# Kernel tuning notes

Measured on AMD Instinct MI355X. Metric: run time of the kernel, lower is better.

## Reference

```python
import jax, jax.numpy as jnp
import numpy as np

L, B, S, H, NH, DH, I, MAXP, NL = 4, 8, 512, 1024, 32, 32, 4096, 512, 20
EPS = 1e-12


def setup_inputs() -> dict:
    key = jax.random.key(0)
    ks = jax.random.split(key, 12)
    sc = 0.02
    w = lambda k, shape: jax.random.normal(k, shape, jnp.float32) * sc
    p = {}
    p['hidden_states'] = jax.random.normal(ks[0], (B, S, H), jnp.float32)
    p['attention_mask'] = jnp.ones((B, S), jnp.float32)
    p['Wq'] = w(ks[1], (L, H, H)); p['bq'] = jnp.zeros((L, H), jnp.float32)
    p['Wk'] = w(ks[2], (L, H, H)); p['bk'] = jnp.zeros((L, H), jnp.float32)
    p['Wv'] = w(ks[3], (L, H, H)); p['bv'] = jnp.zeros((L, H), jnp.float32)
    p['Wo'] = w(ks[4], (L, H, H)); p['bo'] = jnp.zeros((L, H), jnp.float32)
    p['ln1_g'] = jnp.ones((L, H), jnp.float32); p['ln1_b'] = jnp.zeros((L, H), jnp.float32)
    p['W1'] = w(ks[5], (L, H, I)); p['b1'] = jnp.zeros((L, I), jnp.float32)
    p['W2'] = w(ks[6], (L, I, H)); p['b2'] = jnp.zeros((L, H), jnp.float32)
    p['ln2_g'] = jnp.ones((L, H), jnp.float32); p['ln2_b'] = jnp.zeros((L, H), jnp.float32)
    p['rel_emb'] = w(ks[7], (L, 2 * MAXP - 1, DH))
    p['pool_W'] = w(ks[8], (3 * H, H)); p['pool_b'] = jnp.zeros((H,), jnp.float32)
    p['pool_ln_g'] = jnp.ones((H,), jnp.float32); p['pool_ln_b'] = jnp.zeros((H,), jnp.float32)
    p['cls_W'] = w(ks[9], (H, NL)); p['cls_b'] = jnp.zeros((NL,), jnp.float32)
    return p


def _ln(x, g, b):
    mu = jnp.mean(x, -1, keepdims=True)
    var = jnp.mean(jnp.square(x - mu), -1, keepdims=True)
    return (x - mu) * jax.lax.rsqrt(var + EPS) * g + b


def reference(hidden_states, attention_mask, Wq, bq, Wk, bk, Wv, bv, Wo, bo,
              ln1_g, ln1_b, W1, b1, W2, b2, ln2_g, ln2_b, rel_emb,
              pool_W, pool_b, pool_ln_g, pool_ln_b, cls_W, cls_b):
    b, s, h = hidden_states.shape
    # extended additive attention mask (0 -> -1e9)
    mask_add = (1.0 - attention_mask)[:, None, None, :] * -1e9
    pos = jnp.arange(s)
    rel_idx = pos[:, None] - pos[None, :] + MAXP - 1  # [s, s] in [0, 2*MAXP-2]
    x = hidden_states
    for l in range(L):
        heads = lambda t: t.reshape(b, s, NH, DH).transpose(0, 2, 1, 3)
        q = heads(x @ Wq[l] + bq[l])
        k = heads(x @ Wk[l] + bk[l])
        v = heads(x @ Wv[l] + bv[l])
        # learned relative-position bias; note head_size == num_heads by construction
        rel = rel_emb[l][rel_idx].transpose(2, 0, 1)  # [DH==NH, s, s]
        scores = jnp.einsum('bhqd,bhkd->bhqk', q, k) + rel[None]
        scores = scores / np.float32(np.sqrt(DH)) + mask_add
        probs = jax.nn.softmax(scores, axis=-1)
        ctx = jnp.einsum('bhqk,bhkd->bhqd', probs, v).transpose(0, 2, 1, 3).reshape(b, s, h)
        x = _ln(ctx @ Wo[l] + bo[l] + x, ln1_g[l], ln1_b[l])
        inner = jax.nn.gelu(x @ W1[l] + b1[l], approximate=False) @ W2[l] + b2[l]
        x = _ln(x + inner, ln2_g[l], ln2_b[l])
    # AdvancedPooling: mean + max + first token
    m = attention_mask[..., None]
    mean_pool = jnp.sum(x * m, axis=1) / jnp.sum(attention_mask, axis=1, keepdims=True)
    max_pool = jnp.max(x + (1.0 - m) * -1e9, axis=1)
    pooled = jnp.concatenate([mean_pool, max_pool, x[:, 0]], axis=-1)
    pooled = _ln(pooled @ pool_W + pool_b, pool_ln_g, pool_ln_b)
    return pooled @ cls_W + cls_b
```

## Files before the change

kernel.cpp:

```cpp
#include <hip/hip_runtime.h>
#include <math.h>

typedef __attribute__((ext_vector_type(8))) _Float16 f16x8;
typedef __attribute__((ext_vector_type(4))) float f32x4;

__device__ __forceinline__ ushort f2h(float x) {
  union { _Float16 h; ushort u; } c;
  c.h = (_Float16)x;
  return c.u;
}
__device__ __forceinline__ void gl_lds16(const ushort* g, ushort* l) {
  __builtin_amdgcn_global_load_lds(
      (const __attribute__((address_space(1))) unsigned int*)g,
      (__attribute__((address_space(3))) unsigned int*)l, 16, 0, 0);
}
__device__ __forceinline__ f32x4 mfma16(f16x8 a, f16x8 b, f32x4 c) {
  return __builtin_amdgcn_mfma_f32_16x16x32_f16(a, b, c, 0, 0, 0);
}

__device__ __forceinline__ float block_reduce_sum(float v, float* sb) {
#pragma unroll
  for (int o = 32; o > 0; o >>= 1) v += __shfl_down(v, o, 64);
  const int t = threadIdx.x;
  if ((t & 63) == 0) sb[t >> 6] = v;
  __syncthreads();
  v = sb[0] + sb[1] + sb[2] + sb[3];
  __syncthreads();
  return v;
}

__global__ __launch_bounds__(256) void acast(const float* __restrict__ X,
                                             ushort* __restrict__ H, int n4) {
  const int i = blockIdx.x * 256 + threadIdx.x;
  if (i >= n4) return;
  const float4 x = ((const float4*)X)[i];
  ushort4 h;
  h.x = f2h(x.x); h.y = f2h(x.y); h.z = f2h(x.z); h.w = f2h(x.w);
  ((ushort4*)H)[i] = h;
}

__global__ __launch_bounds__(256) void concat3(const float* __restrict__ a,
                                               const float* __restrict__ b,
                                               const float* __restrict__ c,
                                               float* __restrict__ o) {
  const int i = blockIdx.x * 256 + threadIdx.x;
  o[i] = i < 1024 ? a[i] : (i < 2048 ? b[i - 1024] : c[i - 2048]);
}

__global__ __launch_bounds__(256) void wcast_t(const float* __restrict__ W,
                                               ushort* __restrict__ T,
                                               int K, int N) {
  __shared__ float s[32][33];
  const int tx = threadIdx.x & 31, ty = threadIdx.x >> 5;
  const int n0 = blockIdx.x * 32, k0 = blockIdx.y * 32;
#pragma unroll
  for (int i = 0; i < 4; ++i)
    s[ty + i * 8][tx] = W[(size_t)(k0 + ty + i * 8) * N + n0 + tx];
  __syncthreads();
#pragma unroll
  for (int i = 0; i < 4; ++i) {
    const int n = ty + i * 8;
    T[(size_t)(n0 + n) * K + k0 + tx] = f2h(s[tx][n]);
  }
}

template <int EPI, int NF>
__global__ __launch_bounds__(256, NF == 4 ? 2 : 3) void gemm_mfma(
    const ushort* __restrict__ A, const ushort* __restrict__ B,
    const float* __restrict__ bias, const float* __restrict__ res,
    float* __restrict__ C, ushort* __restrict__ O, int M, int N, int K) {
  __shared__ __align__(16) ushort sA[2][4096], sB[2][NF * 1024];
  const int t = threadIdx.x, w = t >> 6, lane = t & 63;
  const int llo = lane & 15, lhi = lane >> 4;
  const int wm = w >> 1, wn = w & 1;

  const int gx = gridDim.x;
  int wg = blockIdx.y * gx + blockIdx.x;
  const int nwg = gx * gridDim.y;
  wg = (wg & 7) * (nwg >> 3) + (wg >> 3);
  const int bm = (wg / gx) * 128, bn = (wg % gx) * (NF * 32);

  const ushort* pA0 = A + (size_t)(bm + lane) * K + w * 8;
  const ushort* pA1 = pA0 + (size_t)64 * K;
  const ushort* pB0 = B + (size_t)(bn + lane) * K + w * 8;
  const ushort* pB1 = (NF == 4) ? pB0 + (size_t)64 * K : pB0;

  auto STAGE = [&](int buf, int k0) {
    gl_lds16(pA0 + k0, &sA[buf][w * 1024]);
    gl_lds16(pA1 + k0, &sA[buf][w * 1024 + 512]);
    if (NF == 4) {
      gl_lds16(pB0 + k0, &sB[buf][w * 1024]);
      gl_lds16(pB1 + k0, &sB[buf][w * 1024 + 512]);
    } else {
      gl_lds16(pB0 + k0, &sB[buf][w * 512]);
    }
  };

  f32x4 acc[4][NF] = {};
  const int NT = K >> 5;
  STAGE(0, 0);
  __syncthreads();
  int cur = 0;
  for (int kt = 0; kt < NT; ++kt) {
    if (kt + 1 < NT) STAGE(cur ^ 1, (kt + 1) << 5);
    f16x8 a[4], bf[NF];
#pragma unroll
    for (int f = 0; f < 4; ++f)
      a[f] = *(const f16x8*)&sA[cur][lhi * 1024 + (wm * 64 + f * 16 + llo) * 8];
#pragma unroll
    for (int f = 0; f < NF; ++f)
      bf[f] = *(const f16x8*)&sB[cur][lhi * (NF * 256) +
                                      (wn * (NF * 16) + f * 16 + llo) * 8];
#pragma unroll
    for (int fm = 0; fm < 4; ++fm)
#pragma unroll
      for (int fn = 0; fn < NF; ++fn)
        acc[fm][fn] = mfma16(a[fm], bf[fn], acc[fm][fn]);
    __syncthreads();
    cur ^= 1;
  }

#pragma unroll
  for (int fm = 0; fm < 4; ++fm) {
    const int row0 = bm + wm * 64 + fm * 16 + lhi * 4;
#pragma unroll
    for (int fn = 0; fn < NF; ++fn) {
      const int col = bn + wn * (NF * 16) + fn * 16 + llo;
      const float bc = bias[col];
      if (EPI == 5) {
        if (col < 2048) {
          const size_t base = (size_t)(col >> 10) * (4096 * 1024) + (col & 1023);
#pragma unroll
          for (int r = 0; r < 4; ++r)
            O[base + (size_t)(row0 + r) * 1024] = f2h(acc[fm][fn][r] + bc);
        } else {
          const int c = col - 2048;
          ushort4 vh;
#pragma unroll
          for (int r = 0; r < 4; ++r) ((ushort*)&vh)[r] = f2h(acc[fm][fn][r] + bc);
          const size_t o = (size_t)8 * 1024 * 1024 +
              ((size_t)(((row0 >> 9) * 32 + (c >> 5)) * 32 + (c & 31))) * 512 +
              (row0 & 511);
          *(ushort4*)(O + o) = vh;
        }
      } else {
#pragma unroll
        for (int r = 0; r < 4; ++r) {
          const size_t o = (size_t)(row0 + r) * N + col;
          float v = acc[fm][fn][r] + bc;
          if (EPI == 2) {
            v += res[o];
            C[o] = v;
          } else {
            v = 0.5f * v * (1.f + erff(v * 0.70710678118654752f));
            O[o] = f2h(v);
          }
        }
      }
    }
  }
}

__global__ __launch_bounds__(512, 2) void attn_mfma(
    const ushort* __restrict__ Qg, const ushort* __restrict__ Kg,
    const ushort* __restrict__ Vg, const float* __restrict__ mask,
    const float* __restrict__ rel_l, ushort* __restrict__ Cg) {
  __shared__ __align__(16) ushort sK[16384], sV[16384];
  __shared__ __align__(16) ushort sP[5120];
  __shared__ float rel_s[1024];
  __shared__ float madd[512];

  const int h = blockIdx.x, b = blockIdx.y, z = blockIdx.z;
  const int t = threadIdx.x, w = t >> 6, lane = t & 63;
  const int llo = lane & 15, lhi = lane >> 4;
  const float SCALE = 0.17677669529663687f;

#pragma unroll
  for (int it = 0; it < 4; ++it) {
    const int task = t + it * 512;
    const int s = task >> 2, oct = task & 3;
    const size_t g = (size_t)(b * 512 + s) * 1024 + h * 32 + oct * 8;
    *(uint4*)&sK[oct * 4096 + s * 8] = *(const uint4*)(Kg + g);
  }
#pragma unroll
  for (int it = 0; it < 4; ++it) {
    const int task = t + it * 512;
    const int d = task >> 6, ko = task & 63;
    const size_t g = (size_t)((b * 32 + h) * 32 + d) * 512 + ko * 8;
    *(uint4*)&sV[ko * 256 + d * 8] = *(const uint4*)(Vg + g);
  }
  for (int i = t; i < 1023; i += 512) rel_s[i] = rel_l[(size_t)i * 32 + h];
  for (int i = t; i < 512; i += 512) madd[i] = (1.f - mask[b * 512 + i]) * -1e9f;
  __syncthreads();

  uint* wP = (uint*)(sP + w * 640 + llo * 40);
  const ushort* rP = sP + w * 640 + llo * 40;

  for (int qt = 0; qt < 2; ++qt) {
    const int q = z * 256 + w * 32 + qt * 16 + llo;
    const size_t qg = (size_t)(b * 512 + q) * 1024 + h * 32 + lhi * 8;
    const f16x8 fQ = *(const f16x8*)(Qg + qg);
    float m = -INFINITY, l = 0.f;
    f32x4 acc0 = {0.f, 0.f, 0.f, 0.f};
    f32x4 acc1 = {0.f, 0.f, 0.f, 0.f};

    for (int kt2 = 0; kt2 < 16; ++kt2) {
      float p[8];
      float tm = -INFINITY;
#pragma unroll
      for (int sub = 0; sub < 2; ++sub) {
        const int kt = kt2 * 2 + sub;
        const f16x8 fK = *(const f16x8*)&sK[lhi * 4096 + (kt * 16 + llo) * 8];
        f32x4 s4 = {0.f, 0.f, 0.f, 0.f};
        s4 = mfma16(fK, fQ, s4);
#pragma unroll
        for (int r = 0; r < 4; ++r) {
          const int k = kt * 16 + lhi * 4 + r;
          const float sv = (s4[r] + rel_s[q - k + 511]) * SCALE + madd[k];
          p[sub * 4 + r] = sv;
          tm = fmaxf(tm, sv);
        }
      }
      tm = fmaxf(tm, __shfl_xor(tm, 16));
      tm = fmaxf(tm, __shfl_xor(tm, 32));
      const float nm = fmaxf(m, tm);
      const float sc = __expf(m - nm);
      float ts = 0.f;
#pragma unroll
      for (int i = 0; i < 8; ++i) {
        p[i] = __expf(p[i] - nm);
        ts += p[i];
      }
      ts += __shfl_xor(ts, 16);
      ts += __shfl_xor(ts, 32);
      l = l * sc + ts;
      m = nm;
      acc0 *= sc;
      acc1 *= sc;
#pragma unroll
      for (int sub = 0; sub < 2; ++sub) {
        wP[sub * 8 + lhi * 2 + 0] =
            (uint)f2h(p[sub * 4 + 0]) | ((uint)f2h(p[sub * 4 + 1]) << 16);
        wP[sub * 8 + lhi * 2 + 1] =
            (uint)f2h(p[sub * 4 + 2]) | ((uint)f2h(p[sub * 4 + 3]) << 16);
      }
      const f16x8 fP = *(const f16x8*)(rP + lhi * 8);
      const int vb = (kt2 * 4 + lhi) * 256;
      const f16x8 fV0 = *(const f16x8*)&sV[vb + llo * 8];
      const f16x8 fV1 = *(const f16x8*)&sV[vb + (16 + llo) * 8];
      acc0 = mfma16(fV0, fP, acc0);
      acc1 = mfma16(fV1, fP, acc1);
    }

    const float invl = 1.f / l;
    const size_t ob = (size_t)(b * 512 + q) * 1024 + h * 32;
    ushort4 oh;
#pragma unroll
    for (int r = 0; r < 4; ++r) ((ushort*)&oh)[r] = f2h(acc0[r] * invl);
    *(ushort4*)(Cg + ob + lhi * 4) = oh;
#pragma unroll
    for (int r = 0; r < 4; ++r) ((ushort*)&oh)[r] = f2h(acc1[r] * invl);
    *(ushort4*)(Cg + ob + 16 + lhi * 4) = oh;
  }
}

__global__ __launch_bounds__(256) void ln_kernel(
    const float* __restrict__ X, const float* __restrict__ g,
    const float* __restrict__ bt, float* __restrict__ out,
    ushort* __restrict__ O) {
  __shared__ float sb[4];
  const int row = blockIdx.x, t = threadIdx.x;
  const float4 x = *(const float4*)&X[(size_t)row * 1024 + t * 4];
  const float s = block_reduce_sum(x.x + x.y + x.z + x.w, sb);
  const float mu = s * (1.f / 1024.f);
  const float dx = x.x - mu, dy = x.y - mu, dz = x.z - mu, dw = x.w - mu;
  const float ss = block_reduce_sum(dx * dx + dy * dy + dz * dz + dw * dw, sb);
  const float rs = rsqrtf(ss * (1.f / 1024.f) + 1e-12f);
  const float4 gv = *(const float4*)&g[t * 4];
  const float4 bv = *(const float4*)&bt[t * 4];
  float4 o;
  o.x = dx * rs * gv.x + bv.x;
  o.y = dy * rs * gv.y + bv.y;
  o.z = dz * rs * gv.z + bv.z;
  o.w = dw * rs * gv.w + bv.w;
  *(float4*)&out[(size_t)row * 1024 + t * 4] = o;
  if (O) {
    ushort4 vh;
    vh.x = f2h(o.x); vh.y = f2h(o.y); vh.z = f2h(o.z); vh.w = f2h(o.w);
    *(ushort4*)&O[(size_t)row * 1024 + t * 4] = vh;
  }
}

__global__ __launch_bounds__(128) void pool_kernel(
    const float* __restrict__ X, const float* __restrict__ mask,
    float* __restrict__ pooled) {
  const int b = blockIdx.y;
  const int col = blockIdx.x * 128 + threadIdx.x;
  float sum = 0.f, mx = -INFINITY, cnt = 0.f;
  for (int s = 0; s < 512; ++s) {
    const float v = X[(size_t)(b * 512 + s) * 1024 + col];
    const float mk = mask[b * 512 + s];
    sum = fmaf(v, mk, sum);
    cnt += mk;
    mx = fmaxf(mx, v + (1.f - mk) * -1e9f);
  }
  pooled[(size_t)b * 3072 + col] = sum / cnt;
  pooled[(size_t)b * 3072 + 1024 + col] = mx;
  pooled[(size_t)b * 3072 + 2048 + col] = X[(size_t)(b * 512) * 1024 + col];
}

__global__ __launch_bounds__(256) void pool_gemm_kernel(
    const float* __restrict__ P, const float* __restrict__ W,
    const float* __restrict__ bias, float* __restrict__ out) {
  const int idx = blockIdx.x * 256 + threadIdx.x;
  const int b = idx >> 10, n = idx & 1023;
  const float* pr = P + (size_t)b * 3072;
  float a = 0.f;
  for (int k = 0; k < 3072; ++k) a = fmaf(pr[k], W[(size_t)k * 1024 + n], a);
  out[idx] = a + bias[n];
}

__global__ __launch_bounds__(64) void cls_kernel(
    const float* __restrict__ X, const float* __restrict__ W,
    const float* __restrict__ bias, float* __restrict__ out) {
  const int b = blockIdx.x, n = threadIdx.x;
  if (n < 20) {
    float a = 0.f;
    for (int k = 0; k < 1024; ++k)
      a = fmaf(X[(size_t)b * 1024 + k], W[(size_t)k * 20 + n], a);
    out[b * 20 + n] = a + bias[n];
  }
}

extern "C" void kernel_launch(void* const* d_in, const int* in_sizes, int n_in,
                              void* d_out, int out_size, void* d_ws, size_t ws_size,
                              hipStream_t stream) {
  const float* hs    = (const float*)d_in[0];
  const float* amask = (const float*)d_in[1];
  const float* Wq    = (const float*)d_in[2];
  const float* bq    = (const float*)d_in[3];
  const float* Wk    = (const float*)d_in[4];
  const float* bk    = (const float*)d_in[5];
  const float* Wv    = (const float*)d_in[6];
  const float* bv    = (const float*)d_in[7];
  const float* Wo    = (const float*)d_in[8];
  const float* bo    = (const float*)d_in[9];
  const float* ln1g  = (const float*)d_in[10];
  const float* ln1b  = (const float*)d_in[11];
  const float* W1    = (const float*)d_in[12];
  const float* b1    = (const float*)d_in[13];
  const float* W2    = (const float*)d_in[14];
  const float* b2    = (const float*)d_in[15];
  const float* ln2g  = (const float*)d_in[16];
  const float* ln2b  = (const float*)d_in[17];
  const float* rel   = (const float*)d_in[18];
  const float* poolW = (const float*)d_in[19];
  const float* poolb = (const float*)d_in[20];
  const float* plng  = (const float*)d_in[21];
  const float* plnb  = (const float*)d_in[22];
  const float* clsW  = (const float*)d_in[23];
  const float* clsb  = (const float*)d_in[24];

  char* W = (char*)d_ws;
  const size_t MB = (size_t)1 << 20;
  const size_t QK = (size_t)4096 * 1024;
  const size_t WP = (size_t)1024 * 1024;
  float* buf_t  = (float*)(W + 0 * MB);
  float* buf_h1 = (float*)(W + 16 * MB);
  float* buf_x  = (float*)(W + 32 * MB);
  ushort* PL  = (ushort*)(W + 48 * MB);
  ushort* CTX = (ushort*)(W + 72 * MB);
  ushort* Xp  = CTX;
  ushort* H1  = (ushort*)(W + 80 * MB);
  ushort* F1  = (ushort*)(W + 88 * MB);
  ushort* Wt  = (ushort*)(W + 120 * MB);
  float* bcat = (float*)(W + 126 * MB);
  float* pooled  = (float*)(W + 127 * MB);
  float* pool_h  = pooled + 8 * 3072;
  float* pool_h2 = pool_h + 8 * 1024;

  const int n4act = (4096 * 1024) / 4;
  const dim3 gQKV(3072 / 128, 32);
  const dim3 gN64(1024 / 64, 32);
  const dim3 gF1(4096 / 128, 32);
  const dim3 wsQ(1024 / 32, 1024 / 32);

  acast<<<n4act / 256, 256, 0, stream>>>(hs, Xp, n4act);

  const float* x_in = hs;
  for (int l = 0; l < 4; ++l) {
    const float* Wq_l = Wq + (size_t)l * 1024 * 1024;
    const float* Wk_l = Wk + (size_t)l * 1024 * 1024;
    const float* Wv_l = Wv + (size_t)l * 1024 * 1024;
    const float* Wo_l = Wo + (size_t)l * 1024 * 1024;
    const float* W1_l = W1 + (size_t)l * 1024 * 4096;
    const float* W2_l = W2 + (size_t)l * 4096 * 1024;

    concat3<<<12, 256, 0, stream>>>(bq + l * 1024, bk + l * 1024, bv + l * 1024, bcat);
    wcast_t<<<wsQ, 256, 0, stream>>>(Wq_l, Wt, 1024, 1024);
    wcast_t<<<wsQ, 256, 0, stream>>>(Wk_l, Wt + WP, 1024, 1024);
    wcast_t<<<wsQ, 256, 0, stream>>>(Wv_l, Wt + 2 * WP, 1024, 1024);
    gemm_mfma<5, 4><<<gQKV, 256, 0, stream>>>(Xp, Wt, bcat, nullptr, nullptr,
                                              PL, 4096, 3072, 1024);

    attn_mfma<<<dim3(32, 8, 2), 512, 0, stream>>>(
        PL, PL + QK, PL + 2 * QK, amask, rel + (size_t)l * 1023 * 32, CTX);

    wcast_t<<<wsQ, 256, 0, stream>>>(Wo_l, Wt, 1024, 1024);
    gemm_mfma<2, 2><<<gN64, 256, 0, stream>>>(CTX, Wt, bo + l * 1024, x_in,
                                              buf_t, nullptr, 4096, 1024, 1024);
    ln_kernel<<<4096, 256, 0, stream>>>(buf_t, ln1g + l * 1024, ln1b + l * 1024,
                                        buf_h1, H1);

    wcast_t<<<dim3(4096 / 32, 1024 / 32), 256, 0, stream>>>(W1_l, Wt, 1024, 4096);
    gemm_mfma<1, 4><<<gF1, 256, 0, stream>>>(H1, Wt, b1 + l * 4096, nullptr,
                                             nullptr, F1, 4096, 4096, 1024);
    wcast_t<<<dim3(1024 / 32, 4096 / 32), 256, 0, stream>>>(W2_l, Wt, 4096, 1024);
    gemm_mfma<2, 2><<<gN64, 256, 0, stream>>>(F1, Wt, b2 + l * 1024, buf_h1,
                                              buf_t, nullptr, 4096, 1024, 4096);
    ln_kernel<<<4096, 256, 0, stream>>>(buf_t, ln2g + l * 1024, ln2b + l * 1024,
                                        buf_x, Xp);
    x_in = buf_x;
  }

  pool_kernel<<<dim3(8, 8), 128, 0, stream>>>(buf_x, amask, pooled);
  pool_gemm_kernel<<<32, 256, 0, stream>>>(pooled, poolW, poolb, pool_h);
  ln_kernel<<<8, 256, 0, stream>>>(pool_h, plng, plnb, pool_h2, nullptr);
  cls_kernel<<<8, 64, 0, stream>>>(pool_h2, clsW, clsb, (float*)d_out);
}
```

Measured before the change: 1.611 ms.

## Split-K wide-tile GEMMs, fuse QKV weight casts, parallelize pooling and classifier head

The GEMM kernel now always uses 128x128 tiles, and the N=1024 projections (Wo and W2) use a 2-way K split whose second partial is summed inside the layernorm kernel. The three QKV weight transposes are merged into one launch. The pooling, pooler GEMM and classifier are split across many more threads with partial-reduction kernels, replacing long serial loops. These changes target low parallelism in the tail kernels and tile reuse in the GEMMs, at the cost of extra fp32 partial buffers and more launches.

```diff
diff --git a/kernel.cpp b/kernel.cpp
--- a/kernel.cpp
+++ b/kernel.cpp
@@ -64,58 +64,75 @@
   }
 }
 
-template <int EPI, int NF>
-__global__ __launch_bounds__(256, NF == 4 ? 2 : 3) void gemm_mfma(
+__global__ __launch_bounds__(256) void wcast_t3(const float* __restrict__ W0,
+                                                const float* __restrict__ W1,
+                                                const float* __restrict__ W2,
+                                                ushort* __restrict__ T) {
+  __shared__ float s[32][33];
+  const float* W = blockIdx.z == 0 ? W0 : (blockIdx.z == 1 ? W1 : W2);
+  ushort* Tp = T + (size_t)blockIdx.z * 1024 * 1024;
+  const int tx = threadIdx.x & 31, ty = threadIdx.x >> 5;
+  const int n0 = blockIdx.x * 32, k0 = blockIdx.y * 32;
+#pragma unroll
+  for (int i = 0; i < 4; ++i)
+    s[ty + i * 8][tx] = W[(size_t)(k0 + ty + i * 8) * 1024 + n0 + tx];
+  __syncthreads();
+#pragma unroll
+  for (int i = 0; i < 4; ++i) {
+    const int n = ty + i * 8;
+    Tp[(size_t)(n0 + n) * 1024 + k0 + tx] = f2h(s[tx][n]);
+  }
+}
+
+template <int EPI, int KSPLIT>
+__global__ __launch_bounds__(256, 2) void gemm_mfma(
     const ushort* __restrict__ A, const ushort* __restrict__ B,
     const float* __restrict__ bias, const float* __restrict__ res,
-    float* __restrict__ C, ushort* __restrict__ O, int M, int N, int K) {
-  __shared__ __align__(16) ushort sA[2][4096], sB[2][NF * 1024];
+    float* __restrict__ C, float* __restrict__ C2, ushort* __restrict__ O,
+    int M, int N, int K) {
+  __shared__ __align__(16) ushort sA[2][4096], sB[2][4096];
   const int t = threadIdx.x, w = t >> 6, lane = t & 63;
   const int llo = lane & 15, lhi = lane >> 4;
   const int wm = w >> 1, wn = w & 1;
+  const int z = (KSPLIT > 1) ? blockIdx.z : 0;
+  const int Ks = K / KSPLIT;
 
   const int gx = gridDim.x;
   int wg = blockIdx.y * gx + blockIdx.x;
   const int nwg = gx * gridDim.y;
   wg = (wg & 7) * (nwg >> 3) + (wg >> 3);
-  const int bm = (wg / gx) * 128, bn = (wg % gx) * (NF * 32);
-
-  const ushort* pA0 = A + (size_t)(bm + lane) * K + w * 8;
+  const int bm = (wg / gx) * 128, bn = (wg % gx) * 128;
+
+  const ushort* pA0 = A + (size_t)(bm + lane) * K + w * 8 + z * Ks;
   const ushort* pA1 = pA0 + (size_t)64 * K;
-  const ushort* pB0 = B + (size_t)(bn + lane) * K + w * 8;
-  const ushort* pB1 = (NF == 4) ? pB0 + (size_t)64 * K : pB0;
+  const ushort* pB0 = B + (size_t)(bn + lane) * K + w * 8 + z * Ks;
+  const ushort* pB1 = pB0 + (size_t)64 * K;
 
   auto STAGE = [&](int buf, int k0) {
     gl_lds16(pA0 + k0, &sA[buf][w * 1024]);
     gl_lds16(pA1 + k0, &sA[buf][w * 1024 + 512]);
-    if (NF == 4) {
-      gl_lds16(pB0 + k0, &sB[buf][w * 1024]);
-      gl_lds16(pB1 + k0, &sB[buf][w * 1024 + 512]);
-    } else {
-      gl_lds16(pB0 + k0, &sB[buf][w * 512]);
-    }
+    gl_lds16(pB0 + k0, &sB[buf][w * 1024]);
+    gl_lds16(pB1 + k0, &sB[buf][w * 1024 + 512]);
   };
 
-  f32x4 acc[4][NF] = {};
-  const int NT = K >> 5;
+  f32x4 acc[4][4] = {};
+  const int NT = Ks >> 5;
   STAGE(0, 0);
   __syncthreads();
   int cur = 0;
   for (int kt = 0; kt < NT; ++kt) {
     if (kt + 1 < NT) STAGE(cur ^ 1, (kt + 1) << 5);
-    f16x8 a[4], bf[NF];
-#pragma unroll
-    for (int f = 0; f < 4; ++f)
+    f16x8 a[4], bfr[4];
+#pragma unroll
+    for (int f = 0; f < 4; ++f) {
       a[f] = *(const f16x8*)&sA[cur][lhi * 1024 + (wm * 64 + f * 16 + llo) * 8];
-#pragma unroll
-    for (int f = 0; f < NF; ++f)
-      bf[f] = *(const f16x8*)&sB[cur][lhi * (NF * 256) +
-                                      (wn * (NF * 16) + f * 16 + llo) * 8];
+      bfr[f] = *(const f16x8*)&sB[cur][lhi * 1024 + (wn * 64 + f * 16 + llo) * 8];
+    }
 #pragma unroll
     for (int fm = 0; fm < 4; ++fm)
 #pragma unroll
-      for (int fn = 0; fn < NF; ++fn)
-        acc[fm][fn] = mfma16(a[fm], bf[fn], acc[fm][fn]);
+      for (int fn = 0; fn < 4; ++fn)
+        acc[fm][fn] = mfma16(a[fm], bfr[fn], acc[fm][fn]);
     __syncthreads();
     cur ^= 1;
   }
@@ -124,8 +141,8 @@
   for (int fm = 0; fm < 4; ++fm) {
     const int row0 = bm + wm * 64 + fm * 16 + lhi * 4;
 #pragma unroll
-    for (int fn = 0; fn < NF; ++fn) {
-      const int col = bn + wn * (NF * 16) + fn * 16 + llo;
+    for (int fn = 0; fn < 4; ++fn) {
+      const int col = bn + wn * 64 + fn * 16 + llo;
       const float bc = bias[col];
       if (EPI == 5) {
         if (col < 2048) {
@@ -143,18 +160,22 @@
               (row0 & 511);
           *(ushort4*)(O + o) = vh;
         }
+      } else if (EPI == 2) {
+#pragma unroll
+        for (int r = 0; r < 4; ++r) {
+          const size_t o = (size_t)(row0 + r) * N + col;
+          if (KSPLIT == 1 || z == 0)
+            C[o] = acc[fm][fn][r] + bc + res[o];
+          else
+            C2[o] = acc[fm][fn][r];
+        }
       } else {
 #pragma unroll
         for (int r = 0; r < 4; ++r) {
           const size_t o = (size_t)(row0 + r) * N + col;
           float v = acc[fm][fn][r] + bc;
-          if (EPI == 2) {
-            v += res[o];
-            C[o] = v;
-          } else {
-            v = 0.5f * v * (1.f + erff(v * 0.70710678118654752f));
-            O[o] = f2h(v);
-          }
+          v = 0.5f * v * (1.f + erff(v * 0.70710678118654752f));
+          O[o] = f2h(v);
         }
       }
     }
@@ -265,12 +286,16 @@
 }
 
 __global__ __launch_bounds__(256) void ln_kernel(
-    const float* __restrict__ X, const float* __restrict__ g,
-    const float* __restrict__ bt, float* __restrict__ out,
-    ushort* __restrict__ O) {
+    const float* __restrict__ X, const float* __restrict__ X2,
+    const float* __restrict__ g, const float* __restrict__ bt,
+    float* __restrict__ out, ushort* __restrict__ O) {
   __shared__ float sb[4];
   const int row = blockIdx.x, t = threadIdx.x;
-  const float4 x = *(const float4*)&X[(size_t)row * 1024 + t * 4];
+  float4 x = *(const float4*)&X[(size_t)row * 1024 + t * 4];
+  if (X2) {
+    const float4 y = *(const float4*)&X2[(size_t)row * 1024 + t * 4];
+    x.x += y.x; x.y += y.y; x.z += y.z; x.w += y.w;
+  }
   const float s = block_reduce_sum(x.x + x.y + x.z + x.w, sb);
   const float mu = s * (1.f / 1024.f);
   const float dx = x.x - mu, dy = x.y - mu, dz = x.z - mu, dw = x.w - mu;
@@ -291,45 +316,98 @@
   }
 }
 
-__global__ __launch_bounds__(128) void pool_kernel(
+__global__ __launch_bounds__(128) void pool_part(
     const float* __restrict__ X, const float* __restrict__ mask,
-    float* __restrict__ pooled) {
-  const int b = blockIdx.y;
-  const int col = blockIdx.x * 128 + threadIdx.x;
+    float* __restrict__ psum, float* __restrict__ pmax,
+    float* __restrict__ pcnt) {
+  const int cb = blockIdx.x, b = blockIdx.y, sb = blockIdx.z;
+  const int col = cb * 128 + threadIdx.x;
   float sum = 0.f, mx = -INFINITY, cnt = 0.f;
-  for (int s = 0; s < 512; ++s) {
+  for (int i = 0; i < 128; ++i) {
+    const int s = sb * 128 + i;
     const float v = X[(size_t)(b * 512 + s) * 1024 + col];
     const float mk = mask[b * 512 + s];
     sum = fmaf(v, mk, sum);
     cnt += mk;
     mx = fmaxf(mx, v + (1.f - mk) * -1e9f);
   }
-  pooled[(size_t)b * 3072 + col] = sum / cnt;
-  pooled[(size_t)b * 3072 + 1024 + col] = mx;
+  psum[(size_t)(sb * 8 + b) * 1024 + col] = sum;
+  pmax[(size_t)(sb * 8 + b) * 1024 + col] = mx;
+  if (cb == 0 && threadIdx.x == 0) pcnt[sb * 8 + b] = cnt;
+}
+
+__global__ __launch_bounds__(256) void pool_fin(
+    const float* __restrict__ X, const float* __restrict__ psum,
+    const float* __restrict__ pmax, const float* __restrict__ pcnt,
+    float* __restrict__ pooled) {
+  const int idx = blockIdx.x * 256 + threadIdx.x;
+  const int b = idx >> 10, col = idx & 1023;
+  float s = 0.f, m = -INFINITY, c = 0.f;
+#pragma unroll
+  for (int sb = 0; sb < 4; ++sb) {
+    s += psum[(size_t)(sb * 8 + b) * 1024 + col];
+    m = fmaxf(m, pmax[(size_t)(sb * 8 + b) * 1024 + col]);
+    c += pcnt[sb * 8 + b];
+  }
+  pooled[(size_t)b * 3072 + col] = s / c;
+  pooled[(size_t)b * 3072 + 1024 + col] = m;
   pooled[(size_t)b * 3072 + 2048 + col] = X[(size_t)(b * 512) * 1024 + col];
 }
 
-__global__ __launch_bounds__(256) void pool_gemm_kernel(
+__global__ __launch_bounds__(256) void pgemm_part(
     const float* __restrict__ P, const float* __restrict__ W,
-    const float* __restrict__ bias, float* __restrict__ out) {
+    float* __restrict__ part) {
+  __shared__ float sP[8][192];
+  __shared__ float sacc[256][9];
+  const int nb = blockIdx.x, kb = blockIdx.y;
+  const int t = threadIdx.x;
+  const int k0 = kb * 192, n0 = nb * 64;
+  for (int i = t; i < 1536; i += 256)
+    sP[i / 192][i % 192] = P[(size_t)(i / 192) * 3072 + k0 + i % 192];
+  __syncthreads();
+  const int n = t & 63, kq = t >> 6;
+  float acc[8] = {};
+  for (int kk = 0; kk < 48; ++kk) {
+    const int k = kq * 48 + kk;
+    const float wv = W[(size_t)(k0 + k) * 1024 + n0 + n];
+#pragma unroll
+    for (int b = 0; b < 8; ++b) acc[b] = fmaf(sP[b][k], wv, acc[b]);
+  }
+#pragma unroll
+  for (int b = 0; b < 8; ++b) sacc[t][b] = acc[b];
+  __syncthreads();
+  for (int p = t; p < 512; p += 256) {
+    const int b = p >> 6, nn = p & 63;
+    const float v = sacc[nn][b] + sacc[64 + nn][b] + sacc[128 + nn][b] +
+                    sacc[192 + nn][b];
+    part[((size_t)kb * 8 + b) * 1024 + n0 + nn] = v;
+  }
+}
+
+__global__ __launch_bounds__(256) void pgemm_fin(
+    const float* __restrict__ part, const float* __restrict__ bias,
+    float* __restrict__ out) {
   const int idx = blockIdx.x * 256 + threadIdx.x;
   const int b = idx >> 10, n = idx & 1023;
-  const float* pr = P + (size_t)b * 3072;
-  float a = 0.f;
-  for (int k = 0; k < 3072; ++k) a = fmaf(pr[k], W[(size_t)k * 1024 + n], a);
-  out[idx] = a + bias[n];
+  float v = bias[n];
+#pragma unroll
+  for (int kb = 0; kb < 16; ++kb) v += part[((size_t)kb * 8 + b) * 1024 + n];
+  out[(size_t)b * 1024 + n] = v;
 }
 
 __global__ __launch_bounds__(64) void cls_kernel(
     const float* __restrict__ X, const float* __restrict__ W,
     const float* __restrict__ bias, float* __restrict__ out) {
-  const int b = blockIdx.x, n = threadIdx.x;
-  if (n < 20) {
-    float a = 0.f;
-    for (int k = 0; k < 1024; ++k)
-      a = fmaf(X[(size_t)b * 1024 + k], W[(size_t)k * 20 + n], a);
-    out[b * 20 + n] = a + bias[n];
-  }
+  const int n = blockIdx.x, b = blockIdx.y, lane = threadIdx.x;
+  float a = 0.f;
+#pragma unroll
+  for (int i = 0; i < 16; ++i) {
+    const int k = lane + i * 64;
+    a = fmaf(X[(size_t)b * 1024 + k], W[(size_t)k * 20 + n], a);
+  }
+#pragma unroll
+  for (int o = 32; o > 0; o >>= 1) a += __shfl_down(a, o, 64);
+  if (lane == 0) out[b * 20 + n] = a + bias[n];
 }
 
 extern "C" void kernel_launch(void* const* d_in, const int* in_sizes, int n_in,
@@ -364,26 +442,31 @@
   char* W = (char*)d_ws;
   const size_t MB = (size_t)1 << 20;
   const size_t QK = (size_t)4096 * 1024;
-  const size_t WP = (size_t)1024 * 1024;
   float* buf_t  = (float*)(W + 0 * MB);
-  float* buf_h1 = (float*)(W + 16 * MB);
-  float* buf_x  = (float*)(W + 32 * MB);
-  ushort* PL  = (ushort*)(W + 48 * MB);
-  ushort* CTX = (ushort*)(W + 72 * MB);
+  float* buf_t2 = (float*)(W + 16 * MB);
+  float* buf_h1 = (float*)(W + 32 * MB);
+  float* buf_x  = (float*)(W + 48 * MB);
+  ushort* PL  = (ushort*)(W + 64 * MB);
+  ushort* CTX = (ushort*)(W + 88 * MB);
   ushort* Xp  = CTX;
-  ushort* H1  = (ushort*)(W + 80 * MB);
-  ushort* F1  = (ushort*)(W + 88 * MB);
-  ushort* Wt  = (ushort*)(W + 120 * MB);
-  float* bcat = (float*)(W + 126 * MB);
-  float* pooled  = (float*)(W + 127 * MB);
+  ushort* H1  = (ushort*)(W + 96 * MB);
+  ushort* F1  = (ushort*)(W + 104 * MB);
+  ushort* Wt  = (ushort*)(W + 136 * MB);
+  float* bcat = (float*)(W + 142 * MB);
+  float* sm   = (float*)(W + 143 * MB);
+  float* pooled  = sm;
   float* pool_h  = pooled + 8 * 3072;
   float* pool_h2 = pool_h + 8 * 1024;
+  float* pcnt    = pool_h2 + 8 * 1024;
+  float* psum    = pcnt + 64;
+  float* pmax    = psum + 4 * 8 * 1024;
+  float* pgpart  = pmax + 4 * 8 * 1024;
 
   const int n4act = (4096 * 1024) / 4;
   const dim3 gQKV(3072 / 128, 32);
-  const dim3 gN64(1024 / 64, 32);
   const dim3 gF1(4096 / 128, 32);
-  const dim3 wsQ(1024 / 32, 1024 / 32);
+  const dim3 gKS(1024 / 128, 32, 2);
+  const dim3 wsQ3(32, 32, 3);
 
   acast<<<n4act / 256, 256, 0, stream>>>(hs, Xp, n4act);
 
@@ -397,34 +480,34 @@
     const float* W2_l = W2 + (size_t)l * 4096 * 1024;
 
     concat3<<<12, 256, 0, stream>>>(bq + l * 1024, bk + l * 1024, bv + l * 1024, bcat);
-    wcast_t<<<wsQ, 256, 0, stream>>>(Wq_l, Wt, 1024, 1024);
-    wcast_t<<<wsQ, 256, 0, stream>>>(Wk_l, Wt + WP, 1024, 1024);
-    wcast_t<<<wsQ, 256, 0, stream>>>(Wv_l, Wt + 2 * WP, 1024, 1024);
-    gemm_mfma<5, 4><<<gQKV, 256, 0, stream>>>(Xp, Wt, bcat, nullptr, nullptr,
-                                              PL, 4096, 3072, 1024);
+    wcast_t3<<<wsQ3, 256, 0, stream>>>(Wq_l, Wk_l, Wv_l, Wt);
+    gemm_mfma<5, 1><<<gQKV, 256, 0, stream>>>(Xp, Wt, bcat, nullptr, nullptr,
+                                              nullptr, PL, 4096, 3072, 1024);
 
     attn_mfma<<<dim3(32, 8, 2), 512, 0, stream>>>(
         PL, PL + QK, PL + 2 * QK, amask, rel + (size_t)l * 1023 * 32, CTX);
 
-    wcast_t<<<wsQ, 256, 0, stream>>>(Wo_l, Wt, 1024, 1024);
-    gemm_mfma<2, 2><<<gN64, 256, 0, stream>>>(CTX, Wt, bo + l * 1024, x_in,
-                                              buf_t, nullptr, 4096, 1024, 1024);
-    ln_kernel<<<4096, 256, 0, stream>>>(buf_t, ln1g + l * 1024, ln1b + l * 1024,
-                                        buf_h1, H1);
+    wcast_t<<<dim3(32, 32), 256, 0, stream>>>(Wo_l, Wt, 1024, 1024);
+    gemm_mfma<2, 2><<<gKS, 256, 0, stream>>>(CTX, Wt, bo + l * 1024, x_in,
+                                             buf_t, buf_t2, nullptr, 4096, 1024, 1024);
+    ln_kernel<<<4096, 256, 0, stream>>>(buf_t, buf_t2, ln1g + l * 1024,
+                                        ln1b + l * 1024, buf_h1, H1);
 
     wcast_t<<<dim3(4096 / 32, 1024 / 32), 256, 0, stream>>>(W1_l, Wt, 1024, 4096);
-    gemm_mfma<1, 4><<<gF1, 256, 0, stream>>>(H1, Wt, b1 + l * 4096, nullptr,
-                                             nullptr, F1, 4096, 4096, 1024);
+    gemm_mfma<1, 1><<<gF1, 256, 0, stream>>>(H1, Wt, b1 + l * 4096, nullptr,
+                                             nullptr, nullptr, F1, 4096, 4096, 1024);
     wcast_t<<<dim3(1024 / 32, 4096 / 32), 256, 0, stream>>>(W2_l, Wt, 4096, 1024);
-    gemm_mfma<2, 2><<<gN64, 256, 0, stream>>>(F1, Wt, b2 + l * 1024, buf_h1,
-                                              buf_t, nullptr, 4096, 1024, 4096);
-    ln_kernel<<<4096, 256, 0, stream>>>(buf_t, ln2g + l * 1024, ln2b + l * 1024,
-                                        buf_x, Xp);
+    gemm_mfma<2, 2><<<gKS, 256, 0, stream>>>(F1, Wt, b2 + l * 1024, buf_h1,
+                                             buf_t, buf_t2, nullptr, 4096, 1024, 4096);
+    ln_kernel<<<4096, 256, 0, stream>>>(buf_t, buf_t2, ln2g + l * 1024,
+                                        ln2b + l * 1024, buf_x, Xp);
     x_in = buf_x;
   }
 
-  pool_kernel<<<dim3(8, 8), 128, 0, stream>>>(buf_x, amask, pooled);
-  pool_gemm_kernel<<<32, 256, 0, stream>>>(pooled, poolW, poolb, pool_h);
-  ln_kernel<<<8, 256, 0, stream>>>(pool_h, plng, plnb, pool_h2, nullptr);
-  cls_kernel<<<8, 64, 0, stream>>>(pool_h2, clsW, clsb, (float*)d_out);
-}
+  pool_part<<<dim3(8, 8, 4), 128, 0, stream>>>(buf_x, amask, psum, pmax, pcnt);
+  pool_fin<<<32, 256, 0, stream>>>(buf_x, psum, pmax, pcnt, pooled);
+  pgemm_part<<<dim3(16, 16), 256, 0, stream>>>(pooled, poolW, pgpart);
+  pgemm_fin<<<32, 256, 0, stream>>>(pgpart, poolb, pool_h);
+  ln_kernel<<<8, 256, 0, stream>>>(pool_h, nullptr, plng, plnb, pool_h2, nullptr);
+  cls_kernel<<<dim3(20, 8), 64, 0, stream>>>(pool_h2, clsW, clsb, (float*)d_out);
+}
```

After: 1.333 ms. 1.21x faster.
